# Optimization experiments

Hardware: AMD Instinct MI355X
Metric: run time of the kernel (lower is better)

Reference implementation:

```python
import jax, jax.numpy as jnp
import numpy as np

D_IN = 128
D_OUT = 128
B, N = 8, 2048
NEG = -9e15


def setup_inputs() -> dict:
    key = jax.random.key(0)
    ks = jax.random.split(key, 7)
    x = jax.random.normal(ks[0], (B, N, D_IN), dtype=jnp.float32)
    adj = jax.random.randint(ks[1], (B, N, N), 0, 2).astype(jnp.float32)
    s_in = 1.0 / np.sqrt(D_IN)
    s_out = 1.0 / np.sqrt(D_OUT)
    s_g = 1.0 / np.sqrt(2 * D_OUT)
    # torch.nn.Linear weights stored pre-transposed: [in, out]
    W_w = jax.random.uniform(ks[2], (D_IN, D_OUT), jnp.float32, -s_in, s_in)
    W_b = jax.random.uniform(ks[3], (D_OUT,), jnp.float32, -s_in, s_in)
    A_w = jax.random.uniform(ks[4], (D_OUT, D_OUT), jnp.float32, -s_out, s_out)
    gate_w = jax.random.uniform(ks[5], (2 * D_OUT, 1), jnp.float32, -s_g, s_g)
    gate_b = jax.random.uniform(ks[6], (1,), jnp.float32, -s_g, s_g)
    return {"x": x, "adj": adj, "W_w": W_w, "W_b": W_b, "A_w": A_w,
            "gate_w": gate_w, "gate_b": gate_b}


def reference(x, adj, W_w, W_b, A_w, gate_w, gate_b):
    h = x @ W_w + W_b                                  # [B,N,D]
    e = jnp.einsum('bnd,bmd->bnm', h @ A_w, h)          # [B,N,N]
    e = e + jnp.swapaxes(e, 1, 2)                       # symmetric
    att = jnp.where(adj > 0, e, NEG)
    att = jax.nn.softmax(att, axis=1)                   # NOTE: dim=1 as in torch code
    att = att * adj
    h_prime = jax.nn.relu(jnp.einsum('bnm,bmd->bnd', att, h))
    coeff = jax.nn.sigmoid(jnp.concatenate([x, h_prime], axis=-1) @ gate_w + gate_b)  # [B,N,1]
    return coeff * x + (1.0 - coeff) * h_prime
```

## Files before the change

### kernel.cpp

```cpp
#include <hip/hip_runtime.h>
#include <hip/hip_bf16.h>

#define B_ 8
#define N_ 2048
#define D_ 128
#define NW_ (N_ / 32)

typedef __bf16 bf16_t;
typedef __bf16 v8bf __attribute__((ext_vector_type(8)));
typedef float  v4f  __attribute__((ext_vector_type(4)));

__global__ __launch_bounds__(256) void k_prep(
    const float* __restrict__ Ww, const float* __restrict__ Aw,
    bf16_t* __restrict__ WT, bf16_t* __restrict__ ST)
{
    int idx = blockIdx.x * 256 + threadIdx.x;
    int o = idx >> 7, i = idx & 127;
    WT[idx] = (bf16_t)Ww[i * D_ + o];
    ST[idx] = (bf16_t)(Aw[i * D_ + o] + Aw[o * D_ + i]);
}

__global__ __launch_bounds__(256) void k_mask(
    const float* __restrict__ adj, unsigned int* __restrict__ mk)
{
    int w = blockIdx.x * 256 + threadIdx.x;
    const float* src = adj + (size_t)w * 32;
    unsigned int bits = 0;
#pragma unroll
    for (int k = 0; k < 8; ++k) {
        float4 f = *(const float4*)(src + k * 4);
        bits |= (f.x > 0.f ? 1u : 0u) << (k * 4 + 0);
        bits |= (f.y > 0.f ? 1u : 0u) << (k * 4 + 1);
        bits |= (f.z > 0.f ? 1u : 0u) << (k * 4 + 2);
        bits |= (f.w > 0.f ? 1u : 0u) << (k * 4 + 3);
    }
    mk[w] = bits;
}

__global__ __launch_bounds__(256) void k_hg(
    const float* __restrict__ x, const float* __restrict__ Wb,
    const bf16_t* __restrict__ WT, const bf16_t* __restrict__ ST,
    bf16_t* __restrict__ hb, bf16_t* __restrict__ gb)
{
    int wave = threadIdx.x >> 6;
    int lane = threadIdx.x & 63;
    int q = lane >> 4;
    int c = lane & 15;
    int nrow0 = blockIdx.x * 64 + wave * 16;

    __shared__ float pw_all[4][16][132];
    float (*pw)[132] = pw_all[wave];

    v8bf ax[4];
#pragma unroll
    for (int kc = 0; kc < 4; ++kc) {
        const float* src = x + (size_t)(nrow0 + c) * D_ + kc * 32 + q * 8;
        float4 f0 = *(const float4*)src;
        float4 f1 = *(const float4*)(src + 4);
        v8bf a;
        a[0]=(bf16_t)f0.x; a[1]=(bf16_t)f0.y; a[2]=(bf16_t)f0.z; a[3]=(bf16_t)f0.w;
        a[4]=(bf16_t)f1.x; a[5]=(bf16_t)f1.y; a[6]=(bf16_t)f1.z; a[7]=(bf16_t)f1.w;
        ax[kc] = a;
    }

#pragma unroll
    for (int ct = 0; ct < 8; ++ct) {
        float bias = Wb[ct * 16 + c];
        v4f acc = {bias, bias, bias, bias};
#pragma unroll
        for (int kc = 0; kc < 4; ++kc) {
            v8bf bw = *(const v8bf*)(WT + (size_t)(ct * 16 + c) * D_ + kc * 32 + q * 8);
            acc = __builtin_amdgcn_mfma_f32_16x16x32_bf16(ax[kc], bw, acc, 0, 0, 0);
        }
#pragma unroll
        for (int r = 0; r < 4; ++r) pw[q * 4 + r][ct * 16 + c] = acc[r];
    }
    __builtin_amdgcn_wave_barrier();

    v8bf ahf[4];
#pragma unroll
    for (int kc = 0; kc < 4; ++kc) {
        v4f p0 = *(const v4f*)&pw[c][kc * 32 + q * 8];
        v4f p1 = *(const v4f*)&pw[c][kc * 32 + q * 8 + 4];
        v8bf a;
#pragma unroll
        for (int j = 0; j < 4; ++j) { a[j] = (bf16_t)p0[j]; a[j+4] = (bf16_t)p1[j]; }
        ahf[kc] = a;
    }
    {
        int row = lane >> 2, seg = lane & 3;
#pragma unroll
        for (int v = 0; v < 4; ++v) {
            v8bf hv;
#pragma unroll
            for (int j = 0; j < 8; ++j) hv[j] = (bf16_t)pw[row][seg * 32 + v * 8 + j];
            *(v8bf*)(hb + (size_t)(nrow0 + row) * D_ + seg * 32 + v * 8) = hv;
        }
    }
    __builtin_amdgcn_wave_barrier();

#pragma unroll
    for (int ct = 0; ct < 8; ++ct) {
        v4f acc = {0.f, 0.f, 0.f, 0.f};
#pragma unroll
        for (int kc = 0; kc < 4; ++kc) {
            v8bf bw = *(const v8bf*)(ST + (size_t)(ct * 16 + c) * D_ + kc * 32 + q * 8);
            acc = __builtin_amdgcn_mfma_f32_16x16x32_bf16(ahf[kc], bw, acc, 0, 0, 0);
        }
#pragma unroll
        for (int r = 0; r < 4; ++r) pw[q * 4 + r][ct * 16 + c] = acc[r];
    }
    __builtin_amdgcn_wave_barrier();
    {
        int row = lane >> 2, seg = lane & 3;
#pragma unroll
        for (int v = 0; v < 4; ++v) {
            v8bf gv;
#pragma unroll
            for (int j = 0; j < 8; ++j) gv[j] = (bf16_t)pw[row][seg * 32 + v * 8 + j];
            *(v8bf*)(gb + (size_t)(nrow0 + row) * D_ + seg * 32 + v * 8) = gv;
        }
    }
}

__global__ __launch_bounds__(256, 2) void k_att(
    const bf16_t* __restrict__ hb, const bf16_t* __restrict__ gb,
    const unsigned int* __restrict__ mk, float* __restrict__ colsum,
    bf16_t* __restrict__ Pt)
{
    int bid = blockIdx.x;
    int b = bid & 7;
    int rest = bid >> 3;
    int nblk = rest >> 3;
    int mgrp = rest & 7;
    int wave = threadIdx.x >> 6;
    int lane = threadIdx.x & 63;
    int q = lane >> 4;
    int c = lane & 15;
    int nbase = nblk * 64;
    int mwav = mgrp * 256 + wave * 64;
    const size_t hgoff = (size_t)b * N_ * D_;
    const unsigned int* mkb = mk + (size_t)b * N_ * NW_;

    __shared__ bf16_t eb_all[4][64][72];
    bf16_t (*eb)[72] = eb_all[wave];

    uint2 wq[4][4];
#pragma unroll
    for (int sub = 0; sub < 4; ++sub)
#pragma unroll
        for (int r = 0; r < 4; ++r) {
            int row = nbase + sub * 16 + q * 4 + r;
            wq[sub][r] = *(const uint2*)(mkb + (size_t)row * NW_ + (mwav >> 5));
        }

    v8bf ag[4][4];
#pragma unroll
    for (int sub = 0; sub < 4; ++sub)
#pragma unroll
        for (int kc = 0; kc < 4; ++kc)
            ag[sub][kc] = *(const v8bf*)(gb + hgoff
                + (size_t)(nbase + sub * 16 + c) * D_ + kc * 32 + q * 8);

#pragma unroll
    for (int t = 0; t < 4; ++t) {
        int mt = mwav + t * 16;
        v8bf bh[4];
#pragma unroll
        for (int kc = 0; kc < 4; ++kc)
            bh[kc] = *(const v8bf*)(hb + hgoff
                + (size_t)(mt + c) * D_ + kc * 32 + q * 8);
        v4f e[4];
#pragma unroll
        for (int sub = 0; sub < 4; ++sub) e[sub] = (v4f){0.f, 0.f, 0.f, 0.f};
#pragma unroll
        for (int kc = 0; kc < 4; ++kc)
#pragma unroll
            for (int sub = 0; sub < 4; ++sub)
                e[sub] = __builtin_amdgcn_mfma_f32_16x16x32_bf16(ag[sub][kc], bh[kc], e[sub], 0, 0, 0);
        unsigned int sh = (unsigned)((t & 1) * 16 + c);
        float cs = 0.f;
#pragma unroll
        for (int sub = 0; sub < 4; ++sub)
#pragma unroll
            for (int r = 0; r < 4; ++r) {
                unsigned int wv = (t >> 1) ? wq[sub][r].y : wq[sub][r].x;
                float ex = __expf(e[sub][r]);
                float pv = ((wv >> sh) & 1u) ? ex : 0.f;
                eb[sub * 16 + q * 4 + r][t * 16 + c] = (bf16_t)pv;
                cs += pv;
            }
        cs += __shfl_xor(cs, 16);
        cs += __shfl_xor(cs, 32);
        if (lane < 16) atomicAdd(&colsum[b * N_ + mt + lane], cs);
    }
    __builtin_amdgcn_wave_barrier();
    int prow = lane >> 3, pseg = lane & 7;
#pragma unroll
    for (int pass = 0; pass < 8; ++pass) {
        int row = pass * 8 + prow;
        v8bf o = *(const v8bf*)&eb[row][pseg * 8];
        *(v8bf*)(Pt + ((size_t)b * N_ + nbase + row) * N_ + mwav + pseg * 8) = o;
    }
}

__global__ __launch_bounds__(256) void k_scaleT(
    const bf16_t* __restrict__ hb, const float* __restrict__ colsum,
    bf16_t* __restrict__ hbTs)
{
    int bid = blockIdx.x;
    int b = bid >> 6;
    int rem = bid & 63;
    int nblk = rem >> 1;
    int dblk = rem & 1;
    int tid = threadIdx.x;
    __shared__ bf16_t sm[64][72];
    __shared__ float sinv[64];
    int n0 = nblk * 64, d0 = dblk * 64;
    int r = tid >> 3, cg = tid & 7;
#pragma unroll
    for (int rr = 0; rr < 2; ++rr) {
        int row = r + rr * 32;
        *(v8bf*)&sm[row][cg * 8] =
            *(const v8bf*)(hb + (size_t)(b * N_ + n0 + row) * D_ + d0 + cg * 8);
    }
    if (tid < 64) {
        float s = colsum[b * N_ + n0 + tid];
        sinv[tid] = (s > 0.f) ? 1.f / s : 0.f;
    }
    __syncthreads();
#pragma unroll
    for (int rr = 0; rr < 2; ++rr) {
        int dr = r + rr * 32;
        v8bf v;
#pragma unroll
        for (int jj = 0; jj < 8; ++jj)
            v[jj] = (bf16_t)((float)sm[cg * 8 + jj][dr] * sinv[cg * 8 + jj]);
        *(v8bf*)(hbTs + (size_t)(b * D_ + d0 + dr) * N_ + n0 + cg * 8) = v;
    }
}

__global__ __launch_bounds__(512, 2) void k_out(
    const bf16_t* __restrict__ Pt, const bf16_t* __restrict__ hbTs,
    const float* __restrict__ x, const float* __restrict__ gw,
    const float* __restrict__ gbias, float* __restrict__ out)
{
    int bid = blockIdx.x;
    int b = bid & 7;
    int nblk = bid >> 3;
    int tid = threadIdx.x;
    int wave = tid >> 6;
    int lane = tid & 63;
    int q = lane >> 4;
    int c = lane & 15;
    int nbase = nblk * 32;
    int nsub = wave & 1;
    int dq = wave >> 1;

    __shared__ float hp[2][16][132];

    const bf16_t* hTb  = hbTs + (size_t)b * D_ * N_;
    const bf16_t* Arow = Pt + (size_t)b * N_ * N_ + (size_t)(nbase + nsub * 16 + c) * N_;
    const bf16_t* Br0  = hTb + (size_t)(dq * 32 + c) * N_;
    const bf16_t* Br1  = hTb + (size_t)(dq * 32 + 16 + c) * N_;

    v4f acc0 = {0.f, 0.f, 0.f, 0.f};
    v4f acc1 = {0.f, 0.f, 0.f, 0.f};
#pragma unroll 4
    for (int ch = 0; ch < 64; ++ch) {
        int mo = ch * 32 + q * 8;
        v8bf pa = *(const v8bf*)(Arow + mo);
        v8bf v0 = *(const v8bf*)(Br0 + mo);
        v8bf v1 = *(const v8bf*)(Br1 + mo);
        acc0 = __builtin_amdgcn_mfma_f32_16x16x32_bf16(pa, v0, acc0, 0, 0, 0);
        acc1 = __builtin_amdgcn_mfma_f32_16x16x32_bf16(pa, v1, acc1, 0, 0, 0);
    }

#pragma unroll
    for (int r = 0; r < 4; ++r) {
        hp[nsub][q * 4 + r][dq * 32 + c]      = acc0[r];
        hp[nsub][q * 4 + r][dq * 32 + 16 + c] = acc1[r];
    }
    __syncthreads();

    int row = tid >> 4;
    int seg = tid & 15;
    size_t g = (size_t)b * N_ + nbase + row;
    const float* xr = x + g * D_ + seg * 8;
    float xv[8], hv[8];
    {
        float4 f0 = *(const float4*)(xr);
        float4 f1 = *(const float4*)(xr + 4);
        xv[0]=f0.x; xv[1]=f0.y; xv[2]=f0.z; xv[3]=f0.w;
        xv[4]=f1.x; xv[5]=f1.y; xv[6]=f1.z; xv[7]=f1.w;
    }
    const float* hrow = &hp[row >> 4][row & 15][seg * 8];
#pragma unroll
    for (int j = 0; j < 8; ++j) hv[j] = fmaxf(hrow[j], 0.f);
    float part = 0.f;
#pragma unroll
    for (int j = 0; j < 8; ++j)
        part += xv[j] * gw[seg * 8 + j] + hv[j] * gw[D_ + seg * 8 + j];
    part += __shfl_xor(part, 1);
    part += __shfl_xor(part, 2);
    part += __shfl_xor(part, 4);
    part += __shfl_xor(part, 8);
    float coeff = 1.f / (1.f + __expf(-(part + gbias[0])));
    float* orow = out + g * D_ + seg * 8;
    float4 o0, o1;
    o0.x = coeff * xv[0] + (1.f - coeff) * hv[0];
    o0.y = coeff * xv[1] + (1.f - coeff) * hv[1];
    o0.z = coeff * xv[2] + (1.f - coeff) * hv[2];
    o0.w = coeff * xv[3] + (1.f - coeff) * hv[3];
    o1.x = coeff * xv[4] + (1.f - coeff) * hv[4];
    o1.y = coeff * xv[5] + (1.f - coeff) * hv[5];
    o1.z = coeff * xv[6] + (1.f - coeff) * hv[6];
    o1.w = coeff * xv[7] + (1.f - coeff) * hv[7];
    *(float4*)(orow)     = o0;
    *(float4*)(orow + 4) = o1;
}

extern "C" void kernel_launch(void* const* d_in, const int* in_sizes, int n_in,
                              void* d_out, int out_size, void* d_ws, size_t ws_size,
                              hipStream_t stream)
{
    const float* x     = (const float*)d_in[0];
    const float* adj   = (const float*)d_in[1];
    const float* Ww    = (const float*)d_in[2];
    const float* Wb    = (const float*)d_in[3];
    const float* Aw    = (const float*)d_in[4];
    const float* gw    = (const float*)d_in[5];
    const float* gbias = (const float*)d_in[6];
    float* out = (float*)d_out;

    char* ws = (char*)d_ws;
    bf16_t* hb     = (bf16_t*)(ws);
    bf16_t* gb     = (bf16_t*)(ws + (4 << 20));
    bf16_t* hbTs   = (bf16_t*)(ws + (8 << 20));
    float*  colsum = (float*)(ws + (12 << 20));
    unsigned int* mkw = (unsigned int*)(ws + (13 << 20));
    bf16_t* Pt     = (bf16_t*)(ws + (17 << 20));
    bf16_t* WT     = (bf16_t*)(ws + (81 << 20));
    bf16_t* ST     = (bf16_t*)(ws + (81 << 20) + (32 << 10));

    hipMemsetAsync(colsum, 0, B_ * N_ * sizeof(float), stream);
    k_prep<<<64, 256, 0, stream>>>(Ww, Aw, WT, ST);
    k_mask<<<B_ * N_ * NW_ / 256, 256, 0, stream>>>(adj, mkw);
    k_hg<<<B_ * N_ / 64, 256, 0, stream>>>(x, Wb, WT, ST, hb, gb);
    k_att<<<2048, 256, 0, stream>>>(hb, gb, mkw, colsum, Pt);
    k_scaleT<<<512, 256, 0, stream>>>(hb, colsum, hbTs);
    k_out<<<512, 512, 0, stream>>>(Pt, hbTs, x, gw, gbias, out);
}
```

Baseline: 352.9 us.

## Enlarge k_out tile to 64 rows per block with four MFMA accumulators per wave

The output GEMM kernel now covers 64 node rows per block instead of 32. Each wave computes a 16x64 output slice with four accumulators, so every loaded P fragment feeds four MFMAs and P is read only twice per block instead of four times. This cuts global/L2 traffic for the P matrix, but halves the grid to 256 blocks and relaxes the launch bound to one block per SIMD set, which lowers occupancy and raises register pressure. The gated epilogue is adjusted to handle 16 columns per thread.

Result: faster. 344.6 us (-2.3%).

```diff
diff --git a/kernel.cpp b/kernel.cpp
--- a/kernel.cpp
+++ b/kernel.cpp
@@ -240,7 +240,7 @@
     }
 }
 
-__global__ __launch_bounds__(512, 2) void k_out(
+__global__ __launch_bounds__(512, 1) void k_out(
     const bf16_t* __restrict__ Pt, const bf16_t* __restrict__ hbTs,
     const float* __restrict__ x, const float* __restrict__ gw,
     const float* __restrict__ gbias, float* __restrict__ out)
@@ -253,71 +253,73 @@
     int lane = tid & 63;
     int q = lane >> 4;
     int c = lane & 15;
-    int nbase = nblk * 32;
-    int nsub = wave & 1;
-    int dq = wave >> 1;
-
-    __shared__ float hp[2][16][132];
+    int nbase = nblk * 64;
+    int nsub = wave & 3;
+    int dh = wave >> 2;
+
+    __shared__ float hp[64][132];
 
     const bf16_t* hTb  = hbTs + (size_t)b * D_ * N_;
     const bf16_t* Arow = Pt + (size_t)b * N_ * N_ + (size_t)(nbase + nsub * 16 + c) * N_;
-    const bf16_t* Br0  = hTb + (size_t)(dq * 32 + c) * N_;
-    const bf16_t* Br1  = hTb + (size_t)(dq * 32 + 16 + c) * N_;
-
-    v4f acc0 = {0.f, 0.f, 0.f, 0.f};
-    v4f acc1 = {0.f, 0.f, 0.f, 0.f};
-#pragma unroll 4
+    const bf16_t* Br[4];
+#pragma unroll
+    for (int dt = 0; dt < 4; ++dt)
+        Br[dt] = hTb + (size_t)(dh * 64 + dt * 16 + c) * N_;
+
+    v4f acc[4];
+#pragma unroll
+    for (int dt = 0; dt < 4; ++dt) acc[dt] = (v4f){0.f, 0.f, 0.f, 0.f};
+
+#pragma unroll 2
     for (int ch = 0; ch < 64; ++ch) {
         int mo = ch * 32 + q * 8;
         v8bf pa = *(const v8bf*)(Arow + mo);
-        v8bf v0 = *(const v8bf*)(Br0 + mo);
-        v8bf v1 = *(const v8bf*)(Br1 + mo);
-        acc0 = __builtin_amdgcn_mfma_f32_16x16x32_bf16(pa, v0, acc0, 0, 0, 0);
-        acc1 = __builtin_amdgcn_mfma_f32_16x16x32_bf16(pa, v1, acc1, 0, 0, 0);
-    }
-
-#pragma unroll
-    for (int r = 0; r < 4; ++r) {
-        hp[nsub][q * 4 + r][dq * 32 + c]      = acc0[r];
-        hp[nsub][q * 4 + r][dq * 32 + 16 + c] = acc1[r];
-    }
+        v8bf vt[4];
+#pragma unroll
+        for (int dt = 0; dt < 4; ++dt)
+            vt[dt] = *(const v8bf*)(Br[dt] + mo);
+#pragma unroll
+        for (int dt = 0; dt < 4; ++dt)
+            acc[dt] = __builtin_amdgcn_mfma_f32_16x16x32_bf16(pa, vt[dt], acc[dt], 0, 0, 0);
+    }
+
+#pragma unroll
+    for (int dt = 0; dt < 4; ++dt)
+#pragma unroll
+        for (int r = 0; r < 4; ++r)
+            hp[nsub * 16 + q * 4 + r][dh * 64 + dt * 16 + c] = acc[dt][r];
     __syncthreads();
 
-    int row = tid >> 4;
-    int seg = tid & 15;
+    int row = tid >> 3;
+    int seg = tid & 7;
     size_t g = (size_t)b * N_ + nbase + row;
-    const float* xr = x + g * D_ + seg * 8;
-    float xv[8], hv[8];
-    {
-        float4 f0 = *(const float4*)(xr);
-        float4 f1 = *(const float4*)(xr + 4);
-        xv[0]=f0.x; xv[1]=f0.y; xv[2]=f0.z; xv[3]=f0.w;
-        xv[4]=f1.x; xv[5]=f1.y; xv[6]=f1.z; xv[7]=f1.w;
-    }
-    const float* hrow = &hp[row >> 4][row & 15][seg * 8];
-#pragma unroll
-    for (int j = 0; j < 8; ++j) hv[j] = fmaxf(hrow[j], 0.f);
+    const float* xr = x + g * D_ + seg * 16;
+    float xv[16], hv[16];
+#pragma unroll
+    for (int j = 0; j < 16; j += 4) {
+        float4 f = *(const float4*)(xr + j);
+        xv[j] = f.x; xv[j+1] = f.y; xv[j+2] = f.z; xv[j+3] = f.w;
+    }
+#pragma unroll
+    for (int j = 0; j < 16; ++j) hv[j] = fmaxf(hp[row][seg * 16 + j], 0.f);
     float part = 0.f;
 #pragma unroll
-    for (int j = 0; j < 8; ++j)
-        part += xv[j] * gw[seg * 8 + j] + hv[j] * gw[D_ + seg * 8 + j];
+    for (int j = 0; j < 16; ++j)
+        part += xv[j] * gw[seg * 16 + j] + hv[j] * gw[D_ + seg * 16 + j];
     part += __shfl_xor(part, 1);
     part += __shfl_xor(part, 2);
     part += __shfl_xor(part, 4);
-    part += __shfl_xor(part, 8);
     float coeff = 1.f / (1.f + __expf(-(part + gbias[0])));
-    float* orow = out + g * D_ + seg * 8;
-    float4 o0, o1;
-    o0.x = coeff * xv[0] + (1.f - coeff) * hv[0];
-    o0.y = coeff * xv[1] + (1.f - coeff) * hv[1];
-    o0.z = coeff * xv[2] + (1.f - coeff) * hv[2];
-    o0.w = coeff * xv[3] + (1.f - coeff) * hv[3];
-    o1.x = coeff * xv[4] + (1.f - coeff) * hv[4];
-    o1.y = coeff * xv[5] + (1.f - coeff) * hv[5];
-    o1.z = coeff * xv[6] + (1.f - coeff) * hv[6];
-    o1.w = coeff * xv[7] + (1.f - coeff) * hv[7];
-    *(float4*)(orow)     = o0;
-    *(float4*)(orow + 4) = o1;
+    float* orow = out + g * D_ + seg * 16;
+#pragma unroll
+    for (int j = 0; j < 16; j += 4) {
+        float4 o;
+        o.x = coeff * xv[j]   + (1.f - coeff) * hv[j];
+        o.y = coeff * xv[j+1] + (1.f - coeff) * hv[j+1];
+        o.z = coeff * xv[j+2] + (1.f - coeff) * hv[j+2];
+        o.w = coeff * xv[j+3] + (1.f - coeff) * hv[j+3];
+        *(float4*)(orow + j) = o;
+    }
 }
 
 extern "C" void kernel_launch(void* const* d_in, const int* in_sizes, int n_in,
@@ -349,5 +351,5 @@
     k_hg<<<B_ * N_ / 64, 256, 0, stream>>>(x, Wb, WT, ST, hb, gb);
     k_att<<<2048, 256, 0, stream>>>(hb, gb, mkw, colsum, Pt);
     k_scaleT<<<512, 256, 0, stream>>>(hb, colsum, hbTs);
-    k_out<<<512, 512, 0, stream>>>(Pt, hbTs, x, gw, gbias, out);
-}
+    k_out<<<256, 512, 0, stream>>>(Pt, hbTs, x, gw, gbias, out);
+}
```
